# Performance work log

Hardware: AMD Instinct MI355X
Metric: run time of the kernel (lower is better)

## Reference

```python
import jax, jax.numpy as jnp
import numpy as np


def setup_inputs() -> dict:
    key = jax.random.key(0)
    ks = jax.random.split(key, 10)
    N, CZ, CH = 512, 128, 128
    s = 1.0 / np.sqrt(CZ)  # keep pre-sigmoid activations in a sane range
    return {
        "z": jax.random.normal(ks[0], (N, N, CZ), dtype=jnp.float32),
        "mask": jnp.ones((N, N, 1), dtype=jnp.float32),
        "weight_ag": jax.random.normal(ks[1], (CH, CZ), dtype=jnp.float32) * s,
        "bias_ag": jax.random.normal(ks[2], (CH,), dtype=jnp.float32) * 0.02,
        "weight_ap": jax.random.normal(ks[3], (CH, CZ), dtype=jnp.float32) * s,
        "bias_ap": jax.random.normal(ks[4], (CH,), dtype=jnp.float32) * 0.02,
        "weight_bg": jax.random.normal(ks[5], (CH, CZ), dtype=jnp.float32) * s,
        "bias_bg": jax.random.normal(ks[6], (CH,), dtype=jnp.float32) * 0.02,
        "weight_bp": jax.random.normal(ks[7], (CH, CZ), dtype=jnp.float32) * s,
        "bias_bp": jax.random.normal(ks[8], (CH,), dtype=jnp.float32) * 0.02,
        "chunk_size": 32,
    }


def _triangle_mul(z, mask, w_ag, b_ag, w_ap, b_ap, w_bg, b_bg, w_bp, b_bp):
    # z: [N, N, c_z]; mask: [N, N, 1]; weights: [c, c_z]
    # a = mask * sigmoid(Linear_ag(z)) * Linear_ap(z)   -> [N, N, c]
    a = mask * jax.nn.sigmoid(jnp.einsum("ijz,cz->ijc", z, w_ag) + b_ag) * (
        jnp.einsum("ijz,cz->ijc", z, w_ap) + b_ap
    )
    b = mask * jax.nn.sigmoid(jnp.einsum("ijz,cz->ijc", z, w_bg) + b_bg) * (
        jnp.einsum("ijz,cz->ijc", z, w_bp) + b_bp
    )
    # outgoing triangle multiplicative combination, channel-first output [c, N, N]
    return jnp.einsum("ikc,jkc->cij", a, b)


def reference(z, mask, weight_ag, bias_ag, weight_ap, bias_ap,
              weight_bg, bias_bg, weight_bp, bias_bp, chunk_size):
    # The torch wrapper chunks the hidden-channel dim of the weights and
    # concatenates the per-chunk [c, N, N] outputs along dim 0. Since every
    # channel is independent, this is mathematically identical to running the
    # full computation at once; we do that (clean, fused form).
    return _triangle_mul(z, mask, weight_ag, bias_ag, weight_ap, bias_ap,
                         weight_bg, bias_bg, weight_bp, bias_bp)
```

## Files before the change

### kernel.cpp

```cpp
#include <hip/hip_runtime.h>
#include <stdint.h>


#define NDIM 512
#define CZ   128
#define CH   128
#define NPOS (NDIM * NDIM)
#define NTILE 16
#define POSB  (NTILE * 32)

typedef __attribute__((ext_vector_type(8))) __bf16 bf16x8;
typedef __attribute__((ext_vector_type(4))) float  f32x4;

__device__ __forceinline__ unsigned short f2bf(float f) {
  unsigned int u = __builtin_bit_cast(unsigned int, f);
  unsigned int r = (u + 0x7fffu + ((u >> 16) & 1u)) >> 16;
  return (unsigned short)r;
}
__device__ __forceinline__ float bf2f_lo(unsigned int u) {
  return __builtin_bit_cast(float, u << 16);
}
__device__ __forceinline__ float bf2f_hi(unsigned int u) {
  return __builtin_bit_cast(float, u & 0xffff0000u);
}

__global__ __launch_bounds__(256) void conv_weights(
    const float* __restrict__ wag, const float* __restrict__ wap,
    const float* __restrict__ wbg, const float* __restrict__ wbp,
    unsigned short* __restrict__ wbf) {
  int idx = blockIdx.x * 256 + threadIdx.x;
  int proj = idx >> 14;
  int rem  = idx & 16383;
  const float* src = (proj == 0) ? wag : (proj == 1) ? wap : (proj == 2) ? wbg : wbp;
  wbf[idx] = f2bf(src[rem]);
}

__global__ __launch_bounds__(512, 4) void proj_fuse(
    const float* __restrict__ z,
    const float* __restrict__ mask,
    const unsigned short* __restrict__ wbf,
    const float* __restrict__ bias_ag, const float* __restrict__ bias_ap,
    const float* __restrict__ bias_bg, const float* __restrict__ bias_bp,
    unsigned short* __restrict__ a_ws,
    unsigned short* __restrict__ b_ws) {
  __shared__ unsigned short zbuf[32 * 136];
  __shared__ unsigned short accb[4 * 128 * 36];

  const int t    = threadIdx.x;
  const int lane = t & 63;
  const int w    = t >> 6;
  const int proj = w & 3;
  const int half = w >> 2;
  const int base = blockIdx.x * POSB;

  const int ml    = lane & 15;
  const int q     = lane >> 4;
  const int koffl = q * 8;

  bf16x8 wfrag[4][4];
#pragma unroll
  for (int ks = 0; ks < 4; ++ks)
#pragma unroll
    for (int ni = 0; ni < 4; ++ni)
      wfrag[ks][ni] = *(const bf16x8*)&wbf[((size_t)proj * CH + half * 64 + ni * 16 + ml) * CZ + ks * 32 + koffl];

  const int pc = t & 7;
  const int cb = t >> 3;
  float bga[2], bpa[2], bgb[2], bpb[2];
#pragma unroll
  for (int it = 0; it < 2; ++it) {
    bga[it] = bias_ag[it * 64 + cb];
    bpa[it] = bias_ap[it * 64 + cb];
    bgb[it] = bias_bg[it * 64 + cb];
    bpb[it] = bias_bp[it * 64 + cb];
  }

#pragma unroll 1
  for (int tt = 0; tt < NTILE; ++tt) {
    const int m0 = base + tt * 32;

#pragma unroll
    for (int it = 0; it < 2; ++it) {
      const int id  = it * 512 + t;
      const int row = id >> 5;
      const int c4  = id & 31;
      const float4 v = *(const float4*)(z + (size_t)(m0 + row) * CZ + c4 * 4);
      unsigned int lo = (unsigned int)f2bf(v.x) | ((unsigned int)f2bf(v.y) << 16);
      unsigned int hi = (unsigned int)f2bf(v.z) | ((unsigned int)f2bf(v.w) << 16);
      *(uint2*)&zbuf[row * 136 + c4 * 4] = make_uint2(lo, hi);
    }
    __syncthreads();

    f32x4 acc[2][4];
#pragma unroll
    for (int mi = 0; mi < 2; ++mi)
#pragma unroll
      for (int ni = 0; ni < 4; ++ni) acc[mi][ni] = (f32x4){0.f, 0.f, 0.f, 0.f};

#pragma unroll
    for (int ks = 0; ks < 4; ++ks) {
      bf16x8 af0 = *(const bf16x8*)&zbuf[(ml)      * 136 + ks * 32 + koffl];
      bf16x8 af1 = *(const bf16x8*)&zbuf[(ml + 16) * 136 + ks * 32 + koffl];
#pragma unroll
      for (int ni = 0; ni < 4; ++ni) {
        acc[0][ni] = __builtin_amdgcn_mfma_f32_16x16x32_bf16(af0, wfrag[ks][ni], acc[0][ni], 0, 0, 0);
        acc[1][ni] = __builtin_amdgcn_mfma_f32_16x16x32_bf16(af1, wfrag[ks][ni], acc[1][ni], 0, 0, 0);
      }
    }

#pragma unroll
    for (int mi = 0; mi < 2; ++mi)
#pragma unroll
      for (int ni = 0; ni < 4; ++ni) {
        const int c    = half * 64 + ni * 16 + ml;
        const int pos0 = mi * 16 + q * 4;
        unsigned int lo = (unsigned int)f2bf(acc[mi][ni][0]) |
                          ((unsigned int)f2bf(acc[mi][ni][1]) << 16);
        unsigned int hi = (unsigned int)f2bf(acc[mi][ni][2]) |
                          ((unsigned int)f2bf(acc[mi][ni][3]) << 16);
        *(uint2*)&accb[((size_t)proj * CH + c) * 36 + pos0] = make_uint2(lo, hi);
      }
    __syncthreads();

    const float4 mv = *(const float4*)(mask + m0 + pc * 4);
    const float mr[4] = {mv.x, mv.y, mv.z, mv.w};
#pragma unroll
    for (int pair = 0; pair < 2; ++pair) {
      const float* bgp = pair ? bgb : bga;
      const float* bpp = pair ? bpb : bpa;
      unsigned short* plane = pair ? b_ws : a_ws;
      const int pg = pair * 2, pp = pg + 1;
#pragma unroll
      for (int it = 0; it < 2; ++it) {
        const int ch = it * 64 + cb;
        uint2 gv = *(const uint2*)&accb[((size_t)pg * CH + ch) * 36 + pc * 4];
        uint2 pv = *(const uint2*)&accb[((size_t)pp * CH + ch) * 36 + pc * 4];
        const float bg = bgp[it];
        const float bp = bpp[it];
        float g[4] = {bf2f_lo(gv.x) + bg, bf2f_hi(gv.x) + bg,
                      bf2f_lo(gv.y) + bg, bf2f_hi(gv.y) + bg};
        float p[4] = {bf2f_lo(pv.x) + bp, bf2f_hi(pv.x) + bp,
                      bf2f_lo(pv.y) + bp, bf2f_hi(pv.y) + bp};
        unsigned short h[4];
#pragma unroll
        for (int r = 0; r < 4; ++r) {
          float s = 1.0f / (1.0f + __expf(-g[r]));
          h[r] = f2bf(mr[r] * s * p[r]);
        }
        *(uint2*)(plane + (size_t)ch * NPOS + m0 + pc * 4) =
            make_uint2((unsigned int)h[0] | ((unsigned int)h[1] << 16),
                       (unsigned int)h[2] | ((unsigned int)h[3] << 16));
      }
    }
    __syncthreads();
  }
}

__global__ __launch_bounds__(256, 3) void tri_gemm(
    const unsigned short* __restrict__ a_ws,
    const unsigned short* __restrict__ b_ws,
    float* __restrict__ out) {
  __shared__ unsigned short sA[128 * 64];
  __shared__ unsigned short sB[128 * 64];

  const int t = threadIdx.x, lane = t & 63, wave = t >> 6;
  const int wm = wave >> 1, wn = wave & 1;

  const int L    = blockIdx.x;
  const int xcd  = L & 7;
  const int slot = L >> 3;
  const int c    = xcd * 16 + (slot >> 4);
  const int tile = slot & 15;
  const int ti   = tile >> 2, tj = tile & 3;
  const int i0 = ti * 128, j0 = tj * 128;

  const unsigned short* Ap = a_ws + (size_t)c * NPOS + (size_t)i0 * NDIM;
  const unsigned short* Bp = b_ws + (size_t)c * NPOS + (size_t)j0 * NDIM;

  f32x4 acc[4][4];
#pragma unroll
  for (int mi = 0; mi < 4; ++mi)
#pragma unroll
    for (int ni = 0; ni < 4; ++ni) acc[mi][ni] = (f32x4){0.f, 0.f, 0.f, 0.f};

  const int srow8  = t >> 3;
  const int schunk = t & 7;
  const int mrow = wm * 64 + (lane & 15);
  const int nrow = wn * 64 + (lane & 15);

  for (int kk = 0; kk < 8; ++kk) {
    const int k0 = kk * 64;
#pragma unroll
    for (int i = 0; i < 4; ++i) {
      const int row = i * 32 + srow8;
      const int kcs = schunk ^ (row & 7);
      __builtin_amdgcn_global_load_lds(
          (const __attribute__((address_space(1))) unsigned int*)(Ap + (size_t)row * NDIM + k0 + kcs * 8),
          (__attribute__((address_space(3))) unsigned int*)&sA[(i * 256 + t) * 8], 16, 0, 0);
      __builtin_amdgcn_global_load_lds(
          (const __attribute__((address_space(1))) unsigned int*)(Bp + (size_t)row * NDIM + k0 + kcs * 8),
          (__attribute__((address_space(3))) unsigned int*)&sB[(i * 256 + t) * 8], 16, 0, 0);
    }
    __syncthreads();

#pragma unroll
    for (int ksub = 0; ksub < 2; ++ksub) {
      const int kc = ksub * 4 + (lane >> 4);
      bf16x8 af[4], bfr[4];
#pragma unroll
      for (int mi = 0; mi < 4; ++mi) {
        const int r = mrow + mi * 16;
        af[mi] = *(const bf16x8*)&sA[r * 64 + ((kc ^ (r & 7)) << 3)];
      }
#pragma unroll
      for (int ni = 0; ni < 4; ++ni) {
        const int r = nrow + ni * 16;
        bfr[ni] = *(const bf16x8*)&sB[r * 64 + ((kc ^ (r & 7)) << 3)];
      }
#pragma unroll
      for (int mi = 0; mi < 4; ++mi)
#pragma unroll
        for (int ni = 0; ni < 4; ++ni)
          acc[mi][ni] = __builtin_amdgcn_mfma_f32_16x16x32_bf16(af[mi], bfr[ni], acc[mi][ni], 0, 0, 0);
    }
    __syncthreads();
  }

  float* O = out + (size_t)c * NPOS + (size_t)i0 * NDIM + j0;
#pragma unroll
  for (int mi = 0; mi < 4; ++mi)
#pragma unroll
    for (int r = 0; r < 4; ++r) {
      const int m = wm * 64 + mi * 16 + (lane >> 4) * 4 + r;
#pragma unroll
      for (int ni = 0; ni < 4; ++ni) {
        const int n = wn * 64 + ni * 16 + (lane & 15);
        O[(size_t)m * NDIM + n] = acc[mi][ni][r];
      }
    }
}

extern "C" void kernel_launch(void* const* d_in, const int* in_sizes, int n_in,
                              void* d_out, int out_size, void* d_ws, size_t ws_size,
                              hipStream_t stream) {
  const float* z    = (const float*)d_in[0];
  const float* mask = (const float*)d_in[1];
  const float* wag  = (const float*)d_in[2];
  const float* bag  = (const float*)d_in[3];
  const float* wap  = (const float*)d_in[4];
  const float* bap  = (const float*)d_in[5];
  const float* wbg  = (const float*)d_in[6];
  const float* bbg  = (const float*)d_in[7];
  const float* wbp  = (const float*)d_in[8];
  const float* bbp  = (const float*)d_in[9];
  float* out = (float*)d_out;

  unsigned short* wbf  = (unsigned short*)d_ws;
  unsigned short* a_ws = (unsigned short*)((char*)d_ws + 131072);
  unsigned short* b_ws = (unsigned short*)((char*)d_ws + 131072 + (size_t)CH * NPOS * 2);

  conv_weights<<<dim3(256), dim3(256), 0, stream>>>(wag, wap, wbg, wbp, wbf);
  proj_fuse<<<dim3(NPOS / POSB), dim3(512), 0, stream>>>(
      z, mask, wbf, bag, bap, bbg, bbp, a_ws, b_ws);
  tri_gemm<<<dim3(2048), dim3(256), 0, stream>>>(a_ws, b_ws, out);
}
```

Before: 388.2 us.

## Double-buffer LDS in both kernels and split projection by gate/proj pair

The projection kernel now runs one block per (position tile, a/b pair) and computes gate and projection in the same wave. The sigmoid-multiply epilogue then runs straight from MFMA registers, with no LDS round trip and no extra barriers. Its z staging and the tri_gemm K-loop both become double-buffered, prefetching the next tile while computing the current one. The cost is that z is read and converted twice (once per pair), and tri_gemm occupancy drops from 3 to 2 blocks because LDS use doubles.

```diff
diff --git a/kernel.cpp b/kernel.cpp
--- a/kernel.cpp
+++ b/kernel.cpp
@@ -16,12 +16,6 @@
   unsigned int u = __builtin_bit_cast(unsigned int, f);
   unsigned int r = (u + 0x7fffu + ((u >> 16) & 1u)) >> 16;
   return (unsigned short)r;
-}
-__device__ __forceinline__ float bf2f_lo(unsigned int u) {
-  return __builtin_bit_cast(float, u << 16);
-}
-__device__ __forceinline__ float bf2f_hi(unsigned int u) {
-  return __builtin_bit_cast(float, u & 0xffff0000u);
 }
 
 __global__ __launch_bounds__(256) void conv_weights(
@@ -35,7 +29,7 @@
   wbf[idx] = f2bf(src[rem]);
 }
 
-__global__ __launch_bounds__(512, 4) void proj_fuse(
+__global__ __launch_bounds__(256, 3) void proj_fuse(
     const float* __restrict__ z,
     const float* __restrict__ mask,
     const unsigned short* __restrict__ wbf,
@@ -43,111 +37,101 @@
     const float* __restrict__ bias_bg, const float* __restrict__ bias_bp,
     unsigned short* __restrict__ a_ws,
     unsigned short* __restrict__ b_ws) {
-  __shared__ unsigned short zbuf[32 * 136];
-  __shared__ unsigned short accb[4 * 128 * 36];
+  __shared__ unsigned short zbuf[2][32 * 136];
 
   const int t    = threadIdx.x;
   const int lane = t & 63;
   const int w    = t >> 6;
-  const int proj = w & 3;
-  const int half = w >> 2;
+  const int pair = blockIdx.y;
   const int base = blockIdx.x * POSB;
 
   const int ml    = lane & 15;
   const int q     = lane >> 4;
   const int koffl = q * 8;
-
-  bf16x8 wfrag[4][4];
+  const int pg = pair * 2, pp = pg + 1;
+
+  bf16x8 wg[4][2], wp[4][2];
 #pragma unroll
   for (int ks = 0; ks < 4; ++ks)
 #pragma unroll
-    for (int ni = 0; ni < 4; ++ni)
-      wfrag[ks][ni] = *(const bf16x8*)&wbf[((size_t)proj * CH + half * 64 + ni * 16 + ml) * CZ + ks * 32 + koffl];
-
-  const int pc = t & 7;
-  const int cb = t >> 3;
-  float bga[2], bpa[2], bgb[2], bpb[2];
-#pragma unroll
-  for (int it = 0; it < 2; ++it) {
-    bga[it] = bias_ag[it * 64 + cb];
-    bpa[it] = bias_ap[it * 64 + cb];
-    bgb[it] = bias_bg[it * 64 + cb];
-    bpb[it] = bias_bp[it * 64 + cb];
+    for (int ni = 0; ni < 2; ++ni) {
+      const int c = w * 32 + ni * 16 + ml;
+      wg[ks][ni] = *(const bf16x8*)&wbf[((size_t)pg * CH + c) * CZ + ks * 32 + koffl];
+      wp[ks][ni] = *(const bf16x8*)&wbf[((size_t)pp * CH + c) * CZ + ks * 32 + koffl];
+    }
+
+  const float* bgp = pair ? bias_bg : bias_ag;
+  const float* bpp = pair ? bias_bp : bias_ap;
+  float bg[2], bp[2];
+#pragma unroll
+  for (int ni = 0; ni < 2; ++ni) {
+    bg[ni] = bgp[w * 32 + ni * 16 + ml];
+    bp[ni] = bpp[w * 32 + ni * 16 + ml];
   }
+  unsigned short* plane = pair ? b_ws : a_ws;
+
+  auto STAGE = [&](int b, int tt) {
+    const int m0s = base + tt * 32;
+#pragma unroll
+    for (int it = 0; it < 4; ++it) {
+      const int id  = it * 256 + t;
+      const int row = id >> 5;
+      const int c4  = id & 31;
+      const float4 v = *(const float4*)(z + (size_t)(m0s + row) * CZ + c4 * 4);
+      unsigned int lo = (unsigned int)f2bf(v.x) | ((unsigned int)f2bf(v.y) << 16);
+      unsigned int hi = (unsigned int)f2bf(v.z) | ((unsigned int)f2bf(v.w) << 16);
+      *(uint2*)&zbuf[b][row * 136 + c4 * 4] = make_uint2(lo, hi);
+    }
+  };
+
+  STAGE(0, 0);
+  __syncthreads();
 
 #pragma unroll 1
   for (int tt = 0; tt < NTILE; ++tt) {
     const int m0 = base + tt * 32;
-
-#pragma unroll
-    for (int it = 0; it < 2; ++it) {
-      const int id  = it * 512 + t;
-      const int row = id >> 5;
-      const int c4  = id & 31;
-      const float4 v = *(const float4*)(z + (size_t)(m0 + row) * CZ + c4 * 4);
-      unsigned int lo = (unsigned int)f2bf(v.x) | ((unsigned int)f2bf(v.y) << 16);
-      unsigned int hi = (unsigned int)f2bf(v.z) | ((unsigned int)f2bf(v.w) << 16);
-      *(uint2*)&zbuf[row * 136 + c4 * 4] = make_uint2(lo, hi);
-    }
-    __syncthreads();
-
-    f32x4 acc[2][4];
+    const int cb = tt & 1;
+    if (tt + 1 < NTILE) STAGE(cb ^ 1, tt + 1);
+
+    f32x4 ag_[2][2], ap_[2][2];
 #pragma unroll
     for (int mi = 0; mi < 2; ++mi)
 #pragma unroll
-      for (int ni = 0; ni < 4; ++ni) acc[mi][ni] = (f32x4){0.f, 0.f, 0.f, 0.f};
+      for (int ni = 0; ni < 2; ++ni) {
+        ag_[mi][ni] = (f32x4){0.f, 0.f, 0.f, 0.f};
+        ap_[mi][ni] = (f32x4){0.f, 0.f, 0.f, 0.f};
+      }
 
 #pragma unroll
     for (int ks = 0; ks < 4; ++ks) {
-      bf16x8 af0 = *(const bf16x8*)&zbuf[(ml)      * 136 + ks * 32 + koffl];
-      bf16x8 af1 = *(const bf16x8*)&zbuf[(ml + 16) * 136 + ks * 32 + koffl];
-#pragma unroll
-      for (int ni = 0; ni < 4; ++ni) {
-        acc[0][ni] = __builtin_amdgcn_mfma_f32_16x16x32_bf16(af0, wfrag[ks][ni], acc[0][ni], 0, 0, 0);
-        acc[1][ni] = __builtin_amdgcn_mfma_f32_16x16x32_bf16(af1, wfrag[ks][ni], acc[1][ni], 0, 0, 0);
-      }
-    }
-
-#pragma unroll
-    for (int mi = 0; mi < 2; ++mi)
-#pragma unroll
-      for (int ni = 0; ni < 4; ++ni) {
-        const int c    = half * 64 + ni * 16 + ml;
-        const int pos0 = mi * 16 + q * 4;
-        unsigned int lo = (unsigned int)f2bf(acc[mi][ni][0]) |
-                          ((unsigned int)f2bf(acc[mi][ni][1]) << 16);
-        unsigned int hi = (unsigned int)f2bf(acc[mi][ni][2]) |
-                          ((unsigned int)f2bf(acc[mi][ni][3]) << 16);
-        *(uint2*)&accb[((size_t)proj * CH + c) * 36 + pos0] = make_uint2(lo, hi);
-      }
-    __syncthreads();
-
-    const float4 mv = *(const float4*)(mask + m0 + pc * 4);
-    const float mr[4] = {mv.x, mv.y, mv.z, mv.w};
-#pragma unroll
-    for (int pair = 0; pair < 2; ++pair) {
-      const float* bgp = pair ? bgb : bga;
-      const float* bpp = pair ? bpb : bpa;
-      unsigned short* plane = pair ? b_ws : a_ws;
-      const int pg = pair * 2, pp = pg + 1;
-#pragma unroll
-      for (int it = 0; it < 2; ++it) {
-        const int ch = it * 64 + cb;
-        uint2 gv = *(const uint2*)&accb[((size_t)pg * CH + ch) * 36 + pc * 4];
-        uint2 pv = *(const uint2*)&accb[((size_t)pp * CH + ch) * 36 + pc * 4];
-        const float bg = bgp[it];
-        const float bp = bpp[it];
-        float g[4] = {bf2f_lo(gv.x) + bg, bf2f_hi(gv.x) + bg,
-                      bf2f_lo(gv.y) + bg, bf2f_hi(gv.y) + bg};
-        float p[4] = {bf2f_lo(pv.x) + bp, bf2f_hi(pv.x) + bp,
-                      bf2f_lo(pv.y) + bp, bf2f_hi(pv.y) + bp};
+      bf16x8 af0 = *(const bf16x8*)&zbuf[cb][(ml)      * 136 + ks * 32 + koffl];
+      bf16x8 af1 = *(const bf16x8*)&zbuf[cb][(ml + 16) * 136 + ks * 32 + koffl];
+#pragma unroll
+      for (int ni = 0; ni < 2; ++ni) {
+        ag_[0][ni] = __builtin_amdgcn_mfma_f32_16x16x32_bf16(af0, wg[ks][ni], ag_[0][ni], 0, 0, 0);
+        ag_[1][ni] = __builtin_amdgcn_mfma_f32_16x16x32_bf16(af1, wg[ks][ni], ag_[1][ni], 0, 0, 0);
+        ap_[0][ni] = __builtin_amdgcn_mfma_f32_16x16x32_bf16(af0, wp[ks][ni], ap_[0][ni], 0, 0, 0);
+        ap_[1][ni] = __builtin_amdgcn_mfma_f32_16x16x32_bf16(af1, wp[ks][ni], ap_[1][ni], 0, 0, 0);
+      }
+    }
+
+#pragma unroll
+    for (int mi = 0; mi < 2; ++mi) {
+      const int pos0 = mi * 16 + q * 4;
+      const float4 mv = *(const float4*)(mask + m0 + pos0);
+      const float mr[4] = {mv.x, mv.y, mv.z, mv.w};
+#pragma unroll
+      for (int ni = 0; ni < 2; ++ni) {
+        const int c = w * 32 + ni * 16 + ml;
         unsigned short h[4];
 #pragma unroll
         for (int r = 0; r < 4; ++r) {
-          float s = 1.0f / (1.0f + __expf(-g[r]));
-          h[r] = f2bf(mr[r] * s * p[r]);
+          const float g = ag_[mi][ni][r] + bg[ni];
+          const float p = ap_[mi][ni][r] + bp[ni];
+          const float s = 1.0f / (1.0f + __expf(-g));
+          h[r] = f2bf(mr[r] * s * p);
         }
-        *(uint2*)(plane + (size_t)ch * NPOS + m0 + pc * 4) =
+        *(uint2*)(plane + (size_t)c * NPOS + m0 + pos0) =
             make_uint2((unsigned int)h[0] | ((unsigned int)h[1] << 16),
                        (unsigned int)h[2] | ((unsigned int)h[3] << 16));
       }
@@ -156,12 +140,12 @@
   }
 }
 
-__global__ __launch_bounds__(256, 3) void tri_gemm(
+__global__ __launch_bounds__(256, 2) void tri_gemm(
     const unsigned short* __restrict__ a_ws,
     const unsigned short* __restrict__ b_ws,
     float* __restrict__ out) {
-  __shared__ unsigned short sA[128 * 64];
-  __shared__ unsigned short sB[128 * 64];
+  __shared__ unsigned short sA[2][128 * 64];
+  __shared__ unsigned short sB[2][128 * 64];
 
   const int t = threadIdx.x, lane = t & 63, wave = t >> 6;
   const int wm = wave >> 1, wn = wave & 1;
@@ -188,7 +172,7 @@
   const int mrow = wm * 64 + (lane & 15);
   const int nrow = wn * 64 + (lane & 15);
 
-  for (int kk = 0; kk < 8; ++kk) {
+  auto STAGE = [&](int b, int kk) {
     const int k0 = kk * 64;
 #pragma unroll
     for (int i = 0; i < 4; ++i) {
@@ -196,12 +180,20 @@
       const int kcs = schunk ^ (row & 7);
       __builtin_amdgcn_global_load_lds(
           (const __attribute__((address_space(1))) unsigned int*)(Ap + (size_t)row * NDIM + k0 + kcs * 8),
-          (__attribute__((address_space(3))) unsigned int*)&sA[(i * 256 + t) * 8], 16, 0, 0);
+          (__attribute__((address_space(3))) unsigned int*)&sA[b][(i * 256 + t) * 8], 16, 0, 0);
       __builtin_amdgcn_global_load_lds(
           (const __attribute__((address_space(1))) unsigned int*)(Bp + (size_t)row * NDIM + k0 + kcs * 8),
-          (__attribute__((address_space(3))) unsigned int*)&sB[(i * 256 + t) * 8], 16, 0, 0);
-    }
-    __syncthreads();
+          (__attribute__((address_space(3))) unsigned int*)&sB[b][(i * 256 + t) * 8], 16, 0, 0);
+    }
+  };
+
+  STAGE(0, 0);
+  __syncthreads();
+
+#pragma unroll 1
+  for (int kk = 0; kk < 8; ++kk) {
+    const int cur = kk & 1;
+    if (kk < 7) STAGE(cur ^ 1, kk + 1);
 
 #pragma unroll
     for (int ksub = 0; ksub < 2; ++ksub) {
@@ -210,12 +202,12 @@
 #pragma unroll
       for (int mi = 0; mi < 4; ++mi) {
         const int r = mrow + mi * 16;
-        af[mi] = *(const bf16x8*)&sA[r * 64 + ((kc ^ (r & 7)) << 3)];
+        af[mi] = *(const bf16x8*)&sA[cur][r * 64 + ((kc ^ (r & 7)) << 3)];
       }
 #pragma unroll
       for (int ni = 0; ni < 4; ++ni) {
         const int r = nrow + ni * 16;
-        bfr[ni] = *(const bf16x8*)&sB[r * 64 + ((kc ^ (r & 7)) << 3)];
+        bfr[ni] = *(const bf16x8*)&sB[cur][r * 64 + ((kc ^ (r & 7)) << 3)];
       }
 #pragma unroll
       for (int mi = 0; mi < 4; ++mi)
@@ -260,7 +252,7 @@
   unsigned short* b_ws = (unsigned short*)((char*)d_ws + 131072 + (size_t)CH * NPOS * 2);
 
   conv_weights<<<dim3(256), dim3(256), 0, stream>>>(wag, wap, wbg, wbp, wbf);
-  proj_fuse<<<dim3(NPOS / POSB), dim3(512), 0, stream>>>(
+  proj_fuse<<<dim3(NPOS / POSB, 2), dim3(256), 0, stream>>>(
       z, mask, wbf, bag, bap, bbg, bbp, a_ws, b_ws);
   tri_gemm<<<dim3(2048), dim3(256), 0, stream>>>(a_ws, b_ws, out);
 }
```

Measured after the change: 382.9 us. About the same (-1.4%).
